# Kernel optimization log

Hardware: AMD Instinct MI355X
Metric: run time of the kernel (lower is better)

Reference implementation:

```python
import jax, jax.numpy as jnp
import numpy as np

EPS = 1e-8

def _conv(x, w, b=None):
    # NCHW conv, stride 1, SAME padding (k=3, pad=1)
    y = jax.lax.conv_general_dilated(x, w, (1, 1), 'SAME',
                                     dimension_numbers=('NCHW', 'OIHW', 'NCHW'))
    if b is not None:
        y = y + b[None, :, None, None]
    return y

def setup_inputs() -> dict:
    key = jax.random.key(0)
    ks = jax.random.split(key, 6)
    B, C, H, W = 512, 1024, 8, 8
    return {
        'x': jax.random.normal(ks[0], (B, C, H, W), jnp.float32),
        'w1_1': jax.random.normal(ks[1], (1, 1, 3, 3), jnp.float32) * 0.1,
        'w5': jax.random.normal(ks[2], (4, 2, 3, 3), jnp.float32) * 0.1,
        'b5': jax.random.normal(ks[3], (4,), jnp.float32) * 0.1,
        'w6': jax.random.normal(ks[4], (1, 4, 3, 3), jnp.float32) * 0.1,
        'b6': jax.random.normal(ks[5], (1,), jnp.float32) * 0.1,
    }

def reference(x, w1_1, w5, b5, w6, b6):
    B, C, H, W = x.shape  # H == W == 8 by module construction
    m = jnp.max(x, axis=1, keepdims=True)  # [B,1,H,W] channel max
    # 2x2 non-overlapping windows, torch unfold layout -> [B,1,(H/2)*(W/2),4]
    win = m.reshape(B, 1, H // 2, 2, W // 2, 2)
    win = win.transpose(0, 1, 2, 4, 3, 5).reshape(B, 1, (H // 2) * (W // 2), 4)
    # probabilistic pooling: clean inf/nan/negatives, sample per window
    winc = jnp.where(jnp.isinf(win) | jnp.isnan(win) | (win < 0), EPS, win)
    skey = jax.random.key(1)
    idx = jax.random.categorical(skey, winc, axis=-1)  # softmax(winc) multinomial
    mo2 = jnp.take_along_axis(winc, idx[..., None], axis=-1)[..., 0]
    mo2 = mo2.reshape(B, 1, H // 2, W // 2)
    # adaptive max/avg pool (4,4) on 8x8 == 2x2 pooling, reuse windows
    mo3 = win.max(axis=-1).reshape(B, 1, H // 2, W // 2)
    ao4 = win.mean(axis=-1).reshape(B, 1, H // 2, W // 2)
    out2 = 0.1 * mo2 + 0.6 * mo3 + 0.3 * ao4
    out2 = _conv(out2, w1_1)  # bias-free 1->1 conv
    out2 = jax.image.resize(out2, (B, 1, H, W), method='bilinear')  # align_corners=False
    out1 = jnp.concatenate([m, out2], axis=1)  # [B,2,H,W]
    gate = jax.nn.sigmoid(_conv(jax.nn.relu(_conv(out1, w5, b5)), w6, b6))  # [B,1,H,W]
    return jax.nn.relu(x * gate)
```

## Files before the change

### kernel.cpp

```cpp
#include <hip/hip_runtime.h>
#include <math.h>

#define C_DIM 1024
#define HW 64
#define NT 1024
#define F4_PER_BATCH 16384
#define PER_T 16
#define EPSV 1e-8f
#define TINYF 1.17549435e-38f

__device__ __forceinline__ void threefry2x32_01(unsigned x0, unsigned x1,
                                                unsigned& o0, unsigned& o1) {
    const unsigned ks0 = 0u, ks1 = 1u, ks2 = 0x1BD11BDBu;
    x0 += ks0; x1 += ks1;
#define TF_R(r) { x0 += x1; x1 = (x1 << (r)) | (x1 >> (32 - (r))); x1 ^= x0; }
    TF_R(13) TF_R(15) TF_R(26) TF_R(6)
    x0 += ks1; x1 += ks2 + 1u;
    TF_R(17) TF_R(29) TF_R(16) TF_R(24)
    x0 += ks2; x1 += ks0 + 2u;
    TF_R(13) TF_R(15) TF_R(26) TF_R(6)
    x0 += ks0; x1 += ks1 + 3u;
    TF_R(17) TF_R(29) TF_R(16) TF_R(24)
    x0 += ks1; x1 += ks2 + 4u;
    TF_R(13) TF_R(15) TF_R(26) TF_R(6)
    x0 += ks2; x1 += ks0 + 5u;
#undef TF_R
    o0 = x0; o1 = x1;
}

__device__ __forceinline__ unsigned jax_random_bits(unsigned n) {
    unsigned o0, o1;
    threefry2x32_01(0u, n, o0, o1);
    return o0 ^ o1;
}

__device__ __forceinline__ bool bad_val(float v) {
    return ((__float_as_uint(v) & 0x7F800000u) == 0x7F800000u) || (v < 0.0f);
}

__global__ __launch_bounds__(NT) void sa_fused_kernel(
    const float* __restrict__ x,
    const float* __restrict__ w11,
    const float* __restrict__ w5,
    const float* __restrict__ b5,
    const float* __restrict__ w6,
    const float* __restrict__ b6,
    float* __restrict__ out)
{
    const int b = blockIdx.x;
    const int t = threadIdx.x;

    const float4* __restrict__ xb = (const float4*)x + (size_t)b * F4_PER_BATCH;
    float4* __restrict__ ob = (float4*)out + (size_t)b * F4_PER_BATCH;

    __shared__ float4 red[16 * 16];
    __shared__ float sm[64];
    __shared__ float sa16[16];
    __shared__ float sb16[16];
    __shared__ float so2[64];
    __shared__ float shid[4 * 64];
    __shared__ __align__(16) float sgate[64];

    float4 xv[PER_T];
    float4 pm = make_float4(-INFINITY, -INFINITY, -INFINITY, -INFINITY);
#pragma unroll
    for (int i = 0; i < PER_T; ++i) {
        xv[i] = xb[t + NT * i];
        pm.x = fmaxf(pm.x, xv[i].x); pm.y = fmaxf(pm.y, xv[i].y);
        pm.z = fmaxf(pm.z, xv[i].z); pm.w = fmaxf(pm.w, xv[i].w);
    }
#pragma unroll
    for (int off = 16; off <= 32; off <<= 1) {
        pm.x = fmaxf(pm.x, __shfl_xor(pm.x, off, 64));
        pm.y = fmaxf(pm.y, __shfl_xor(pm.y, off, 64));
        pm.z = fmaxf(pm.z, __shfl_xor(pm.z, off, 64));
        pm.w = fmaxf(pm.w, __shfl_xor(pm.w, off, 64));
    }
    const int wv = t >> 6, lane = t & 63;
    if (lane < 16) red[wv * 16 + lane] = pm;
    __syncthreads();

    if (t < 64) {
        if (t < 16) {
            float4 a = red[t];
#pragma unroll
            for (int w = 1; w < 16; ++w) {
                float4 o = red[w * 16 + t];
                a.x = fmaxf(a.x, o.x); a.y = fmaxf(a.y, o.y);
                a.z = fmaxf(a.z, o.z); a.w = fmaxf(a.w, o.w);
            }
            sm[t * 4 + 0] = a.x; sm[t * 4 + 1] = a.y;
            sm[t * 4 + 2] = a.z; sm[t * 4 + 3] = a.w;
        }
        __builtin_amdgcn_wave_barrier();

        if (t < 16) {
            int h2 = t >> 2, w2 = t & 3;
            float win[4], winc[4], sg[4];
#pragma unroll
            for (int j = 0; j < 4; ++j) {
                int hh = 2 * h2 + (j >> 1), ww = 2 * w2 + (j & 1);
                float v = sm[hh * 8 + ww];
                win[j] = v;
                winc[j] = bad_val(v) ? EPSV : v;
                unsigned n = (unsigned)(b * 64 + t * 4 + j);
                unsigned bits = jax_random_bits(n);
                float f = __uint_as_float(0x3F800000u | (bits >> 9)) - 1.0f;
                float u = fmaxf(TINYF, f + TINYF);
                sg[j] = -logf(-logf(u));
            }
            int idx = 0;
            float best = winc[0] + sg[0];
#pragma unroll
            for (int j = 1; j < 4; ++j) {
                float s = winc[j] + sg[j];
                if (s > best) { best = s; idx = j; }
            }
            float mo2 = winc[idx];
            float mo3 = fmaxf(fmaxf(win[0], win[1]), fmaxf(win[2], win[3]));
            float ssum = ((win[0] + win[1]) + win[2]) + win[3];
            float ao4 = ssum * 0.25f;
            sa16[t] = 0.1f * mo2 + 0.6f * mo3 + 0.3f * ao4;
        }
        __builtin_amdgcn_wave_barrier();

        if (t < 16) {
            int i = t >> 2, j = t & 3;
            float acc = 0.0f;
#pragma unroll
            for (int dy = -1; dy <= 1; ++dy) {
                int yy = i + dy;
                if (yy < 0 || yy > 3) continue;
#pragma unroll
                for (int dx = -1; dx <= 1; ++dx) {
                    int xx = j + dx;
                    if (xx < 0 || xx > 3) continue;
                    acc += sa16[yy * 4 + xx] * w11[(dy + 1) * 3 + (dx + 1)];
                }
            }
            sb16[t] = acc;
        }
        __builtin_amdgcn_wave_barrier();

        {
            int y = t >> 3, xx2 = t & 7;
            float sy = (y + 0.5f) * 0.5f - 0.5f;
            float sx = (xx2 + 0.5f) * 0.5f - 0.5f;
            float fy = fminf(fmaxf(sy, 0.0f), 3.0f);
            float fx = fminf(fmaxf(sx, 0.0f), 3.0f);
            int iy0 = (int)floorf(fy); int iy1 = min(iy0 + 1, 3); float ry = fy - (float)iy0;
            int ix0 = (int)floorf(fx); int ix1 = min(ix0 + 1, 3); float rx = fx - (float)ix0;
            float v00 = sb16[iy0 * 4 + ix0], v01 = sb16[iy0 * 4 + ix1];
            float v10 = sb16[iy1 * 4 + ix0], v11 = sb16[iy1 * 4 + ix1];
            float top = v00 * (1.0f - rx) + v01 * rx;
            float bot = v10 * (1.0f - rx) + v11 * rx;
            so2[t] = top * (1.0f - ry) + bot * ry;
        }
        __builtin_amdgcn_wave_barrier();

        {
            int y = t >> 3, x2 = t & 7;
            float a0 = b5[0], a1 = b5[1], a2 = b5[2], a3 = b5[3];
#pragma unroll
            for (int dy = -1; dy <= 1; ++dy) {
                int yy = y + dy;
                if (yy < 0 || yy > 7) continue;
#pragma unroll
                for (int dx = -1; dx <= 1; ++dx) {
                    int xx = x2 + dx;
                    if (xx < 0 || xx > 7) continue;
                    float i0 = sm[yy * 8 + xx];
                    float i1 = so2[yy * 8 + xx];
                    int kk = (dy + 1) * 3 + (dx + 1);
                    a0 += i0 * w5[0 * 18 + kk] + i1 * w5[0 * 18 + 9 + kk];
                    a1 += i0 * w5[1 * 18 + kk] + i1 * w5[1 * 18 + 9 + kk];
                    a2 += i0 * w5[2 * 18 + kk] + i1 * w5[2 * 18 + 9 + kk];
                    a3 += i0 * w5[3 * 18 + kk] + i1 * w5[3 * 18 + 9 + kk];
                }
            }
            shid[0 * 64 + t] = fmaxf(a0, 0.0f);
            shid[1 * 64 + t] = fmaxf(a1, 0.0f);
            shid[2 * 64 + t] = fmaxf(a2, 0.0f);
            shid[3 * 64 + t] = fmaxf(a3, 0.0f);
        }
        __builtin_amdgcn_wave_barrier();

        {
            int y = t >> 3, x2 = t & 7;
            float acc = b6[0];
#pragma unroll
            for (int dy = -1; dy <= 1; ++dy) {
                int yy = y + dy;
                if (yy < 0 || yy > 7) continue;
#pragma unroll
                for (int dx = -1; dx <= 1; ++dx) {
                    int xx = x2 + dx;
                    if (xx < 0 || xx > 7) continue;
                    int kk = (dy + 1) * 3 + (dx + 1);
                    int p = yy * 8 + xx;
                    acc += shid[0 * 64 + p] * w6[0 + kk]
                         + shid[1 * 64 + p] * w6[9 + kk]
                         + shid[2 * 64 + p] * w6[18 + kk]
                         + shid[3 * 64 + p] * w6[27 + kk];
                }
            }
            sgate[t] = 1.0f / (1.0f + expf(-acc));
        }
    }
    __syncthreads();

    const float4 gv = ((const float4*)sgate)[t & 15];
#pragma unroll
    for (int i = 0; i < PER_T; ++i) {
        float4 v = xv[i];
        float4 o;
        o.x = fmaxf(v.x * gv.x, 0.0f);
        o.y = fmaxf(v.y * gv.y, 0.0f);
        o.z = fmaxf(v.z * gv.z, 0.0f);
        o.w = fmaxf(v.w * gv.w, 0.0f);
        ob[t + NT * i] = o;
    }
}

extern "C" void kernel_launch(void* const* d_in, const int* in_sizes, int n_in,
                              void* d_out, int out_size, void* d_ws, size_t ws_size,
                              hipStream_t stream) {
    const float* x   = (const float*)d_in[0];
    const float* w11 = (const float*)d_in[1];
    const float* w5  = (const float*)d_in[2];
    const float* b5  = (const float*)d_in[3];
    const float* w6  = (const float*)d_in[4];
    const float* b6  = (const float*)d_in[5];
    float* out  = (float*)d_out;

    int B = in_sizes[0] / (C_DIM * HW);
    sa_fused_kernel<<<dim3(B), dim3(NT), 0, stream>>>(x, w11, w5, b5, w6, b6, out);
}
```

Before: 247.7 us.

## Parallelize gate prologue across wave lanes, pin loaded registers, use nontemporal stores

The single-wave gate computation is spread across all 64 lanes: the cross-wave max reduction is split into four partial groups merged with shuffles, and each lane now computes one window element's Gumbel sample, with the argmax, max and sum combined through lane shuffles instead of serial loops over 16 lanes. Empty asm constraints pin the loaded x values in registers so the compiler cannot re-load or reorder them. Output stores become nontemporal to avoid polluting cache. Risks include changed tie-breaking semantics in the argmax and extra register pressure.

```diff
diff --git a/kernel.cpp b/kernel.cpp
--- a/kernel.cpp
+++ b/kernel.cpp
@@ -8,6 +8,13 @@
 #define PER_T 16
 #define EPSV 1e-8f
 #define TINYF 1.17549435e-38f
+
+typedef float f32x4_t __attribute__((ext_vector_type(4)));
+
+__device__ __forceinline__ void keepf(float& v) { asm volatile("" : "+v"(v)); }
+__device__ __forceinline__ void keep4(float4& v) {
+    keepf(v.x); keepf(v.y); keepf(v.z); keepf(v.w);
+}
 
 __device__ __forceinline__ void threefry2x32_01(unsigned x0, unsigned x1,
                                                 unsigned& o0, unsigned& o1) {
@@ -70,6 +77,9 @@
         pm.z = fmaxf(pm.z, xv[i].z); pm.w = fmaxf(pm.w, xv[i].w);
     }
 #pragma unroll
+    for (int i = 0; i < PER_T; ++i) keep4(xv[i]);
+
+#pragma unroll
     for (int off = 16; off <= 32; off <<= 1) {
         pm.x = fmaxf(pm.x, __shfl_xor(pm.x, off, 64));
         pm.y = fmaxf(pm.y, __shfl_xor(pm.y, off, 64));
@@ -81,46 +91,56 @@
     __syncthreads();
 
     if (t < 64) {
-        if (t < 16) {
-            float4 a = red[t];
-#pragma unroll
-            for (int w = 1; w < 16; ++w) {
-                float4 o = red[w * 16 + t];
+        {
+            int g = t & 15, set = t >> 4;
+            float4 a = red[(set * 4 + 0) * 16 + g];
+#pragma unroll
+            for (int w = 1; w < 4; ++w) {
+                float4 o = red[(set * 4 + w) * 16 + g];
                 a.x = fmaxf(a.x, o.x); a.y = fmaxf(a.y, o.y);
                 a.z = fmaxf(a.z, o.z); a.w = fmaxf(a.w, o.w);
             }
-            sm[t * 4 + 0] = a.x; sm[t * 4 + 1] = a.y;
-            sm[t * 4 + 2] = a.z; sm[t * 4 + 3] = a.w;
-        }
-        __builtin_amdgcn_wave_barrier();
-
-        if (t < 16) {
-            int h2 = t >> 2, w2 = t & 3;
-            float win[4], winc[4], sg[4];
-#pragma unroll
-            for (int j = 0; j < 4; ++j) {
-                int hh = 2 * h2 + (j >> 1), ww = 2 * w2 + (j & 1);
-                float v = sm[hh * 8 + ww];
-                win[j] = v;
-                winc[j] = bad_val(v) ? EPSV : v;
-                unsigned n = (unsigned)(b * 64 + t * 4 + j);
-                unsigned bits = jax_random_bits(n);
-                float f = __uint_as_float(0x3F800000u | (bits >> 9)) - 1.0f;
-                float u = fmaxf(TINYF, f + TINYF);
-                sg[j] = -logf(-logf(u));
-            }
-            int idx = 0;
-            float best = winc[0] + sg[0];
-#pragma unroll
-            for (int j = 1; j < 4; ++j) {
-                float s = winc[j] + sg[j];
-                if (s > best) { best = s; idx = j; }
-            }
-            float mo2 = winc[idx];
-            float mo3 = fmaxf(fmaxf(win[0], win[1]), fmaxf(win[2], win[3]));
-            float ssum = ((win[0] + win[1]) + win[2]) + win[3];
-            float ao4 = ssum * 0.25f;
-            sa16[t] = 0.1f * mo2 + 0.6f * mo3 + 0.3f * ao4;
+#pragma unroll
+            for (int off = 16; off <= 32; off <<= 1) {
+                a.x = fmaxf(a.x, __shfl_xor(a.x, off, 64));
+                a.y = fmaxf(a.y, __shfl_xor(a.y, off, 64));
+                a.z = fmaxf(a.z, __shfl_xor(a.z, off, 64));
+                a.w = fmaxf(a.w, __shfl_xor(a.w, off, 64));
+            }
+            if (t < 16) {
+                sm[t * 4 + 0] = a.x; sm[t * 4 + 1] = a.y;
+                sm[t * 4 + 2] = a.z; sm[t * 4 + 3] = a.w;
+            }
+        }
+        __builtin_amdgcn_wave_barrier();
+
+        {
+            int w = t >> 2, j = t & 3;
+            int hh = 2 * (w >> 2) + (j >> 1), ww = 2 * (w & 3) + (j & 1);
+            float v = sm[hh * 8 + ww];
+            float wc = bad_val(v) ? EPSV : v;
+            unsigned bits = jax_random_bits((unsigned)(b * 64 + t));
+            float f = __uint_as_float(0x3F800000u | (bits >> 9)) - 1.0f;
+            float u = fmaxf(TINYF, f + TINYF);
+            float sg = -logf(-logf(u));
+            float s = wc + sg;
+            int bi = j;
+            float bwc = wc;
+            float mx = v;
+            float ssum = v;
+#pragma unroll
+            for (int m = 1; m <= 2; m <<= 1) {
+                float s2   = __shfl_xor(s, m, 64);
+                int   bi2  = __shfl_xor(bi, m, 64);
+                float bwc2 = __shfl_xor(bwc, m, 64);
+                float mx2  = __shfl_xor(mx, m, 64);
+                float ss2  = __shfl_xor(ssum, m, 64);
+                bool take = (s2 > s) || (s2 == s && bi2 < bi);
+                if (take) { s = s2; bi = bi2; bwc = bwc2; }
+                mx = fmaxf(mx, mx2);
+                ssum += ss2;
+            }
+            if (j == 0) sa16[w] = 0.1f * bwc + 0.6f * mx + 0.3f * (ssum * 0.25f);
         }
         __builtin_amdgcn_wave_barrier();
 
@@ -213,12 +233,12 @@
 #pragma unroll
     for (int i = 0; i < PER_T; ++i) {
         float4 v = xv[i];
-        float4 o;
+        f32x4_t o;
         o.x = fmaxf(v.x * gv.x, 0.0f);
         o.y = fmaxf(v.y * gv.y, 0.0f);
         o.z = fmaxf(v.z * gv.z, 0.0f);
         o.w = fmaxf(v.w * gv.w, 0.0f);
-        ob[t + NT * i] = o;
+        __builtin_nontemporal_store(o, (f32x4_t*)&ob[t + NT * i]);
     }
 }
 
```

After: 243.2 us, median of 3. About the same (-1.8%).
